# Optimization experiments

Measured on AMD Instinct MI355X. Metric: run time of the kernel, lower is better.

## Reference

```python
import jax, jax.numpy as jnp
import numpy as np

N, D, H, DH = 8192, 512, 8, 64          # seq len, model dim, heads, head dim
NF = int(DH * math_log) if False else 266  # nb_features = int(64 * ln(64)) = 266
EPS = 1e-4                               # performer softmax-kernel eps
LN_EPS = 1e-5


def layernorm(x, g, b):
    mu = x.mean(-1, keepdims=True)
    var = ((x - mu) ** 2).mean(-1, keepdims=True)
    return (x - mu) * jax.lax.rsqrt(var + LN_EPS) * g + b


def softmax_kernel(data, proj, is_query):
    # data: [b,h,n,dh], proj: [nf,dh] -> phi(data): [b,h,n,nf]
    dnorm = DH ** -0.25
    ratio = NF ** -0.5
    dd = jnp.einsum('bhnd,jd->bhnj', data * dnorm, proj)
    diag = (data ** 2).sum(-1, keepdims=True) * 0.5 * (dnorm ** 2)
    if is_query:
        m = jnp.max(dd, axis=-1, keepdims=True)
    else:
        m = jnp.max(dd, axis=(-1, -2), keepdims=True)
    return ratio * (jnp.exp(dd - diag - m) + EPS)


def setup_inputs() -> dict:
    key = jax.random.key(0)
    ks = jax.random.split(key, 10)
    s = 0.02
    return {
        'x': jax.random.normal(ks[0], (N, D), jnp.float32),
        'proj': jax.random.normal(ks[1], (NF, DH), jnp.float32),
        'ln1_g': jnp.ones((D,), jnp.float32), 'ln1_b': jnp.zeros((D,), jnp.float32),
        'wq': jax.random.normal(ks[2], (D, D), jnp.float32) * s,
        'wk': jax.random.normal(ks[3], (D, D), jnp.float32) * s,
        'wv': jax.random.normal(ks[4], (D, D), jnp.float32) * s,
        'wo': jax.random.normal(ks[5], (D, D), jnp.float32) * s,
        'wo_b': jnp.zeros((D,), jnp.float32),
        'ln2_g': jnp.ones((D,), jnp.float32), 'ln2_b': jnp.zeros((D,), jnp.float32),
        'w1': jax.random.normal(ks[6], (D, 4 * D), jnp.float32) * s,
        'b1': jnp.zeros((4 * D,), jnp.float32),
        'w2': jax.random.normal(ks[7], (4 * D, D), jnp.float32) * s,
        'b2': jnp.zeros((D,), jnp.float32),
    }


def reference(x, proj, ln1_g, ln1_b, wq, wk, wv, wo, wo_b, ln2_g, ln2_b, w1, b1, w2, b2):
    xb = x[None]                                     # [1,N,D] (the unsqueeze(0))
    # --- PreLN FAVOR+ self-attention ---
    h = layernorm(xb, ln1_g, ln1_b)
    def split_heads(t):
        return t.reshape(1, N, H, DH).transpose(0, 2, 1, 3)   # [1,H,N,DH]
    q = split_heads(h @ wq)
    k = split_heads(h @ wk)
    v = split_heads(h @ wv)
    qp = softmax_kernel(q, proj, True)               # [1,H,N,NF]
    kp = softmax_kernel(k, proj, False)              # [1,H,N,NF]
    # non-causal linear attention
    context = jnp.einsum('bhnj,bhnd->bhjd', kp, v)   # [1,H,NF,DH]
    d_inv = 1.0 / jnp.einsum('bhnj,bhj->bhn', qp, kp.sum(axis=2))
    attn = jnp.einsum('bhnj,bhjd->bhnd', qp, context) * d_inv[..., None]
    attn = attn.transpose(0, 2, 1, 3).reshape(1, N, D)
    xb = xb + attn @ wo + wo_b
    # --- PreLN feed-forward (GELU, mult=4) ---
    h2 = layernorm(xb, ln2_g, ln2_b)
    xb = xb + jax.nn.gelu(h2 @ w1 + b1) @ w2 + b2
    return xb[0]                                     # squeeze -> [N,D]
```

## Files before the change

### kernel.cpp

```cpp
#include <hip/hip_runtime.h>
#include <math.h>


typedef __attribute__((ext_vector_type(8))) short bf16x8;
typedef __attribute__((ext_vector_type(4))) float f32x4;

#define N_SEQ 8192
#define DMODEL 512
#define DQKV 1536
#define NHEAD 8
#define DHEAD 64
#define NF 266
#define NFP 320
#define PEPS 1e-4f
#define LNEPS 1e-5f
#define RATIO 0.06131393694f

__device__ __forceinline__ unsigned short f2bf(float f) {
  unsigned u = __float_as_uint(f);
  u += 0x7FFFu + ((u >> 16) & 1u);
  return (unsigned short)(u >> 16);
}
__device__ __forceinline__ float bf2f(unsigned short b) {
  return __uint_as_float(((unsigned)b) << 16);
}
__device__ __forceinline__ unsigned enc_f32(float f) {
  unsigned i = __float_as_uint(f);
  return (i & 0x80000000u) ? ~i : (i | 0x80000000u);
}
__device__ __forceinline__ float dec_f32(unsigned u) {
  return (u & 0x80000000u) ? __uint_as_float(u & 0x7FFFFFFFu) : __uint_as_float(~u);
}

__device__ __forceinline__ void g2l16(const void* g, void* l) {
  __builtin_amdgcn_global_load_lds(
      (const __attribute__((address_space(1))) void*)g,
      (__attribute__((address_space(3))) void*)l, 16, 0, 0);
}

template <int N>
__device__ __forceinline__ void wait_vmcnt() {
  if constexpr (N == 0) asm volatile("s_waitcnt vmcnt(0)" ::: "memory");
  else if constexpr (N == 6) asm volatile("s_waitcnt vmcnt(6)" ::: "memory");
  else if constexpr (N == 12) asm volatile("s_waitcnt vmcnt(12)" ::: "memory");
}
__device__ __forceinline__ void wait_lgkm0() {
  asm volatile("s_waitcnt lgkmcnt(0)" ::: "memory");
}


__global__ __launch_bounds__(256) void prep_kernel(
    const float* __restrict__ wq, const float* __restrict__ wk,
    const float* __restrict__ wv, const float* __restrict__ wo,
    const float* __restrict__ w1, const float* __restrict__ w2,
    const float* __restrict__ proj,
    unsigned short* __restrict__ wtqkv, unsigned short* __restrict__ wot,
    unsigned short* __restrict__ w1t, unsigned short* __restrict__ w2t,
    unsigned short* __restrict__ pb, unsigned* __restrict__ mk) {
  int bid = blockIdx.x;
  if (bid < 3072) {
    const float* src; unsigned short* dst; int R, C, base;
    if (bid < 256)       { src = wq; dst = wtqkv;          R = 512;  C = 512;  base = 0; }
    else if (bid < 512)  { src = wk; dst = wtqkv + 262144; R = 512;  C = 512;  base = 256; }
    else if (bid < 768)  { src = wv; dst = wtqkv + 524288; R = 512;  C = 512;  base = 512; }
    else if (bid < 1024) { src = wo; dst = wot;            R = 512;  C = 512;  base = 768; }
    else if (bid < 2048) { src = w1; dst = w1t;            R = 512;  C = 2048; base = 1024; }
    else                 { src = w2; dst = w2t;            R = 2048; C = 512;  base = 2048; }
    int lb = bid - base;
    int nbx = C / 32;
    int c0 = (lb % nbx) * 32, r0 = (lb / nbx) * 32;
    __shared__ float tile[32][33];
    int tx = threadIdx.x & 31, ty = threadIdx.x >> 5;
    #pragma unroll
    for (int i = ty; i < 32; i += 8)
      tile[i][tx] = src[(long)(r0 + i) * C + c0 + tx];
    __syncthreads();
    #pragma unroll
    for (int i = ty; i < 32; i += 8)
      dst[(long)(c0 + i) * R + r0 + tx] = f2bf(tile[tx][i]);
  } else if (bid < 3152) {
    int id = (bid - 3072) * 256 + threadIdx.x;
    int j = id >> 6;
    pb[id] = (j < NF) ? f2bf(proj[(long)j * 64 + (id & 63)] * 0.35355339059327373f)
                      : (unsigned short)0;
  } else {
    if (threadIdx.x < NHEAD) mk[threadIdx.x] = 0x007FFFFFu;
  }
}


__global__ __launch_bounds__(256) void ln_kernel(const float* __restrict__ x,
                                                 const float* __restrict__ g,
                                                 const float* __restrict__ b,
                                                 unsigned short* __restrict__ out) {
  __shared__ float sred[4];
  int row = blockIdx.x, t = threadIdx.x;
  float2 v = ((const float2*)(x + (long)row * DMODEL))[t];
  float s = v.x + v.y;
  #pragma unroll
  for (int m = 32; m >= 1; m >>= 1) s += __shfl_xor(s, m);
  if ((t & 63) == 0) sred[t >> 6] = s;
  __syncthreads();
  float mu = (sred[0] + sred[1] + sred[2] + sred[3]) * (1.0f / DMODEL);
  __syncthreads();
  float d0 = v.x - mu, d1 = v.y - mu;
  float q = d0 * d0 + d1 * d1;
  #pragma unroll
  for (int m = 32; m >= 1; m >>= 1) q += __shfl_xor(q, m);
  if ((t & 63) == 0) sred[t >> 6] = q;
  __syncthreads();
  float var = (sred[0] + sred[1] + sred[2] + sred[3]) * (1.0f / DMODEL);
  float inv = rsqrtf(var + LNEPS);
  int c = t * 2;
  unsigned short o0 = f2bf(d0 * inv * g[c] + b[c]);
  unsigned short o1 = f2bf(d1 * inv * g[c + 1] + b[c + 1]);
  ((unsigned*)(out + (long)row * DMODEL))[t] = ((unsigned)o1 << 16) | o0;
}

enum { EPI_BF16 = 0, EPI_BIAS_RES_F32 = 2, EPI_BIAS_GELU = 3, EPI_QKV = 4 };


template <int BM, int BN, int WM, int WN, int EPI>
__global__ __launch_bounds__(256) void gemm_kernel(
    const unsigned short* __restrict__ A, int lda,
    const unsigned short* __restrict__ Bt, int ldb,
    void* __restrict__ Cv, int ldc,
    int K,
    const float* __restrict__ bias,
    const float* __restrict__ res, int ldr,
    unsigned short* __restrict__ vt) {
  static_assert((BM / WM) * (BN / WN) == 4, "need 4 waves");
  constexpr int MR = WM / 16, NR = WN / 16;
  constexpr int WNN = BN / WN;
  constexpr int AIT = BM * 8 / 256;
  constexpr int BIT = BN * 8 / 256;
  constexpr int S = AIT + BIT;
  const int tid = threadIdx.x;
  const int wave = tid >> 6, lane = tid & 63;
  const int lr = lane & 15, lg = lane >> 4;
  const int wr = wave / WNN, wc = wave % WNN;
  const int m0 = blockIdx.x * BM, n0 = blockIdx.y * BN;

  __shared__ uint4 a_s[2][BM * 8];
  __shared__ uint4 b_s[2][BN * 8];

  const unsigned short* asrc[AIT];
  #pragma unroll
  for (int e = 0; e < AIT; ++e) {
    int chunk = e * 256 + tid;
    int r = chunk >> 3, c = chunk & 7;
    asrc[e] = A + (long)(m0 + r) * lda + (c ^ (r & 7)) * 8;
  }
  const unsigned short* bsrc[BIT];
  #pragma unroll
  for (int e = 0; e < BIT; ++e) {
    int chunk = e * 256 + tid;
    int r = chunk >> 3, c = chunk & 7;
    bsrc[e] = Bt + (long)(n0 + r) * ldb + (c ^ (r & 7)) * 8;
  }
  const int wbase = tid & 192;

  f32x4 acc[MR][NR] = {};

  auto stage = [&](int buf, int t) {
    #pragma unroll
    for (int e = 0; e < AIT; ++e)
      g2l16(asrc[e] + t * 64, &a_s[buf][e * 256 + wbase]);
    #pragma unroll
    for (int e = 0; e < BIT; ++e)
      g2l16(bsrc[e] + t * 64, &b_s[buf][e * 256 + wbase]);
  };
  auto compute = [&](int buf) {
    #pragma unroll
    for (int ks = 0; ks < 2; ++ks) {
      bf16x8 af[MR], bv[NR];
      #pragma unroll
      for (int i = 0; i < MR; ++i) {
        int r = wr * WM + i * 16 + lr;
        af[i] = *(const bf16x8*)&a_s[buf][r * 8 + ((ks * 4 + lg) ^ (r & 7))];
      }
      #pragma unroll
      for (int j = 0; j < NR; ++j) {
        int r = wc * WN + j * 16 + lr;
        bv[j] = *(const bf16x8*)&b_s[buf][r * 8 + ((ks * 4 + lg) ^ (r & 7))];
      }
      #pragma unroll
      for (int i = 0; i < MR; ++i)
        #pragma unroll
        for (int j = 0; j < NR; ++j)
          acc[i][j] = __builtin_amdgcn_mfma_f32_16x16x32_bf16(af[i], bv[j], acc[i][j], 0, 0, 0);
    }
  };

  const int NT = K >> 6;
  stage(0, 0);
  stage(1, 1);
  wait_vmcnt<S>();
  __builtin_amdgcn_s_barrier();

  int cur = 0;
  for (int t = 0; t < NT; ++t) {
    compute(cur);
    if (t + 1 < NT) {
      wait_lgkm0();
      __builtin_amdgcn_s_barrier();
      if (t + 2 < NT) {
        stage(cur, t + 2);
        wait_vmcnt<S>();
      } else {
        wait_vmcnt<0>();
      }
      __builtin_amdgcn_s_barrier();
    }
    cur ^= 1;
  }

  #pragma unroll
  for (int i = 0; i < MR; ++i) {
    #pragma unroll
    for (int j = 0; j < NR; ++j) {
      int gn = n0 + wc * WN + j * 16 + lr;
      int gm0 = m0 + wr * WM + i * 16 + lg * 4;
      if (EPI == EPI_QKV && gn >= 1024) {
        int d = gn - 1024;
        uint2 u;
        u.x = (unsigned)f2bf(acc[i][j][0]) | ((unsigned)f2bf(acc[i][j][1]) << 16);
        u.y = (unsigned)f2bf(acc[i][j][2]) | ((unsigned)f2bf(acc[i][j][3]) << 16);
        *(uint2*)(vt + (long)d * N_SEQ + gm0) = u;
        continue;
      }
      #pragma unroll
      for (int rg = 0; rg < 4; ++rg) {
        int gm = gm0 + rg;
        float v = acc[i][j][rg];
        if (EPI == EPI_BF16 || EPI == EPI_QKV) {
          ((unsigned short*)Cv)[(long)gm * ldc + gn] = f2bf(v);
        } else if (EPI == EPI_BIAS_RES_F32) {
          v += bias[gn] + res[(long)gm * ldr + gn];
          ((float*)Cv)[(long)gm * ldc + gn] = v;
        } else if (EPI == EPI_BIAS_GELU) {
          v += bias[gn];
          float t3 = 0.7978845608028654f * (v + 0.044715f * v * v * v);
          v = v / (1.0f + __expf(-2.0f * t3));
          ((unsigned short*)Cv)[(long)gm * ldc + gn] = f2bf(v);
        }
      }
    }
  }
}


__global__ __launch_bounds__(256) void kmax_kernel(
    const unsigned short* __restrict__ Kp,
    const unsigned short* __restrict__ pb,
    unsigned* __restrict__ mk) {
  const int tid = threadIdx.x;
  const int wave = tid >> 6, lane = tid & 63;
  const int lr = lane & 15, lg = lane >> 4;
  const int h = blockIdx.z;
  const int m0 = blockIdx.x * 64;

  __shared__ uint4 a_s4[512];
  __shared__ uint4 b_s4[2560];
  __shared__ float sred[4];

  const unsigned short* Aq = Kp + (long)m0 * DQKV + h * DHEAD;
  const int wbase = tid & 192;

  #pragma unroll
  for (int e = 0; e < 2; ++e) {
    int chunk = e * 256 + tid;
    int r = chunk >> 3, c = chunk & 7;
    g2l16(Aq + (long)r * DQKV + (c ^ (r & 7)) * 8, a_s4 + e * 256 + wbase);
  }
  #pragma unroll
  for (int e = 0; e < 10; ++e) {
    int chunk = e * 256 + tid;
    int r = chunk >> 3, c = chunk & 7;
    g2l16(pb + (long)r * DHEAD + (c ^ (r & 7)) * 8, b_s4 + e * 256 + wbase);
  }
  __syncthreads();

  f32x4 acc[17] = {};
  #pragma unroll
  for (int ks = 0; ks < 2; ++ks) {
    int rA = wave * 16 + lr;
    bf16x8 af = *(const bf16x8*)&a_s4[rA * 8 + ((ks * 4 + lg) ^ (rA & 7))];
    #pragma unroll
    for (int j = 0; j < 17; ++j) {
      int rB = j * 16 + lr;
      bf16x8 bv = *(const bf16x8*)&b_s4[rB * 8 + ((ks * 4 + lg) ^ (rB & 7))];
      acc[j] = __builtin_amdgcn_mfma_f32_16x16x32_bf16(af, bv, acc[j], 0, 0, 0);
    }
  }

  float m = -3.0e38f;
  #pragma unroll
  for (int j = 0; j < 17; ++j) {
    bool valid = (j < 16) || (lr < 10);
    if (valid) {
      #pragma unroll
      for (int rg = 0; rg < 4; ++rg) m = fmaxf(m, acc[j][rg]);
    }
  }
  #pragma unroll
  for (int s = 1; s < 64; s <<= 1) m = fmaxf(m, __shfl_xor(m, s));
  if (lane == 0) sred[wave] = m;
  __syncthreads();
  if (tid == 0) {
    float mm = fmaxf(fmaxf(sred[0], sred[1]), fmaxf(sred[2], sred[3]));
    atomicMax(&mk[h], enc_f32(mm));
  }
}


__global__ __launch_bounds__(256) void ctx_fused_kernel(
    const unsigned short* __restrict__ Kp,
    const unsigned short* __restrict__ pb,
    const unsigned short* __restrict__ vT,
    const unsigned* __restrict__ mk,
    float* __restrict__ part,
    float* __restrict__ kspart) {
  const int tid = threadIdx.x;
  const int wave = tid >> 6, lane = tid & 63;
  const int lr = lane & 15, lg = lane >> 4;
  const int kc = blockIdx.x, h = blockIdx.y;
  const int wbase = tid & 192;

  __shared__ uint4 smem[7168];
  uint4* pbs = smem;
  auto kbuf = [&](int b) { return smem + 2560 + b * 512; };
  auto vbuf = [&](int b) { return smem + 3584 + b * 512; };
  uint4* Pt = smem + 4608;

  #pragma unroll
  for (int e = 0; e < 10; ++e) {
    int chunk = e * 256 + tid;
    int r = chunk >> 3, c = chunk & 7;
    g2l16(pb + (long)r * DHEAD + (c ^ (r & 7)) * 8, pbs + e * 256 + wbase);
  }

  auto stage_kv = [&](int b, int sub) {
    int n0 = kc * 256 + sub * 64;
    #pragma unroll
    for (int e = 0; e < 2; ++e) {
      int chunk = e * 256 + tid;
      int r = chunk >> 3, c = chunk & 7;
      g2l16(Kp + (long)(n0 + r) * DQKV + h * DHEAD + (c ^ (r & 7)) * 8,
            kbuf(b) + e * 256 + wbase);
      g2l16(vT + ((long)h * DHEAD + r) * N_SEQ + n0 + (c ^ (r & 7)) * 8,
            vbuf(b) + e * 256 + wbase);
    }
  };

  const float mh = dec_f32(mk[h]);
  f32x4 acc2[2][10] = {};
  float colacc[20];
  #pragma unroll
  for (int j = 0; j < 20; ++j) colacc[j] = 0.f;

  const int wr = wave >> 1, wc = wave & 1;

  stage_kv(0, 0);
  for (int sub = 0; sub < 4; ++sub) {
    const int cur = sub & 1;
    __syncthreads();
    if (sub + 1 < 4) stage_kv(cur ^ 1, sub + 1);

    f32x4 acc[20] = {};
    float qs = 0.f;
    #pragma unroll
    for (int ks = 0; ks < 2; ++ks) {
      int rA = wave * 16 + lr;
      bf16x8 af = *(const bf16x8*)&kbuf(cur)[rA * 8 + ((ks * 4 + lg) ^ (rA & 7))];
      #pragma unroll
      for (int i = 0; i < 8; ++i) {
        float f = bf2f((unsigned short)af[i]);
        qs += f * f;
      }
      #pragma unroll
      for (int j = 0; j < 20; ++j) {
        int rB = j * 16 + lr;
        bf16x8 bv = *(const bf16x8*)&pbs[rB * 8 + ((ks * 4 + lg) ^ (rB & 7))];
        acc[j] = __builtin_amdgcn_mfma_f32_16x16x32_bf16(af, bv, acc[j], 0, 0, 0);
      }
    }
    qs += __shfl_xor(qs, 16);
    qs += __shfl_xor(qs, 32);
    float dg[4];
    #pragma unroll
    for (int rg = 0; rg < 4; ++rg) dg[rg] = 0.0625f * __shfl(qs, lg * 4 + rg);

    __syncthreads();

    unsigned short* Ptu = (unsigned short*)Pt;
    const int nrow = wave * 16 + lg * 4;
    #pragma unroll
    for (int j = 0; j < 20; ++j) {
      int colj = j * 16 + lr;
      #pragma unroll
      for (int rg = 0; rg < 4; ++rg) {
        float v = 0.f;
        if (colj < NF) v = RATIO * (__expf(acc[j][rg] - dg[rg] - mh) + PEPS);
        colacc[j] += v;
        int nr = nrow + rg;
        int idx = ((colj * 8 + ((nr >> 3) ^ (colj & 7))) << 3) + (nr & 7);
        Ptu[idx] = f2bf(v);
      }
    }
    __syncthreads();

    #pragma unroll
    for (int ks = 0; ks < 2; ++ks) {
      bf16x8 af[2], bv[10];
      #pragma unroll
      for (int i = 0; i < 2; ++i) {
        int r = wr * 32 + i * 16 + lr;
        af[i] = *(const bf16x8*)&vbuf(cur)[r * 8 + ((ks * 4 + lg) ^ (r & 7))];
      }
      #pragma unroll
      for (int j = 0; j < 10; ++j) {
        int r = wc * 160 + j * 16 + lr;
        bv[j] = *(const bf16x8*)&Pt[r * 8 + ((ks * 4 + lg) ^ (r & 7))];
      }
      #pragma unroll
      for (int i = 0; i < 2; ++i)
        #pragma unroll
        for (int j = 0; j < 10; ++j)
          acc2[i][j] = __builtin_amdgcn_mfma_f32_16x16x32_bf16(af[i], bv[j], acc2[i][j], 0, 0, 0);
    }
  }

  float* pbase = part + ((long)(h * 32 + kc)) * 64 * NFP;
  #pragma unroll
  for (int i = 0; i < 2; ++i) {
    #pragma unroll
    for (int j = 0; j < 10; ++j) {
      int gn = wc * 160 + j * 16 + lr;
      #pragma unroll
      for (int rg = 0; rg < 4; ++rg) {
        int gm = wr * 32 + i * 16 + lg * 4 + rg;
        pbase[(long)gm * NFP + gn] = acc2[i][j][rg];
      }
    }
  }

  __syncthreads();
  float* kls = (float*)Pt;
  #pragma unroll
  for (int j = 0; j < 20; ++j) {
    float cs = colacc[j];
    cs += __shfl_xor(cs, 16);
    cs += __shfl_xor(cs, 32);
    if (lg == 0) kls[wave * NFP + j * 16 + lr] = cs;
  }
  __syncthreads();
  for (int c0 = tid; c0 < NFP; c0 += 256) {
    kspart[((long)(h * 32 + kc)) * NFP + c0] =
        kls[c0] + kls[NFP + c0] + kls[2 * NFP + c0] + kls[3 * NFP + c0];
  }
}


__global__ void ctx_reduce_kernel(const float* __restrict__ part,
                                  const float* __restrict__ kspart,
                                  unsigned short* __restrict__ ctxpad) {
  int i = blockIdx.x * 256 + threadIdx.x;
  int h = i / (96 * NFP);
  int rem = i % (96 * NFP);
  int r = rem / NFP, j = rem % NFP;
  float s = 0.f;
  if (r < 64) {
    #pragma unroll 4
    for (int kc = 0; kc < 32; ++kc)
      s += part[((long)(h * 32 + kc)) * 64 * NFP + r * NFP + j];
  } else if (r == 64) {
    #pragma unroll 4
    for (int kc = 0; kc < 32; ++kc)
      s += kspart[((long)(h * 32 + kc)) * NFP + j];
  }
  ctxpad[i] = f2bf(s);
}


__global__ __launch_bounds__(256) void attn_fused_kernel(
    const unsigned short* __restrict__ Qp,
    const unsigned short* __restrict__ pb,
    const unsigned short* __restrict__ ctxpad,
    unsigned short* __restrict__ attn) {
  const int tid = threadIdx.x;
  const int wave = tid >> 6, lane = tid & 63;
  const int lr = lane & 15, lg = lane >> 4;
  const int h = blockIdx.z;
  const int m0 = blockIdx.x * 64;
  const int wbase = tid & 192;

  __shared__ uint4 smem[4096];
  auto sbuf = [&](int b) { return smem + b * 768; };
  uint4* Pf = smem + 1536;

  const unsigned short* Aq = Qp + (long)m0 * DQKV + h * DHEAD;
  const unsigned short* Ch = ctxpad + (long)h * 96 * NFP;

  auto stage_ctx = [&](int b, int kk) {
    #pragma unroll
    for (int e = 0; e < 3; ++e) {
      int chunk = e * 256 + tid;
      int r = chunk >> 3, c = chunk & 7;
      g2l16(Ch + (long)r * NFP + kk * 64 + (c ^ (r & 7)) * 8, sbuf(b) + e * 256 + wbase);
    }
  };

  #pragma unroll
  for (int e = 0; e < 2; ++e) {
    int chunk = e * 256 + tid;
    int r = chunk >> 3, c = chunk & 7;
    g2l16(Aq + (long)r * DQKV + (c ^ (r & 7)) * 8, sbuf(0) + e * 256 + wbase);
  }
  #pragma unroll
  for (int e = 0; e < 10; ++e) {
    int chunk = e * 256 + tid;
    int r = chunk >> 3, c = chunk & 7;
    g2l16(pb + (long)r * DHEAD + (c ^ (r & 7)) * 8, Pf + e * 256 + wbase);
  }
  __syncthreads();

  f32x4 acc[20] = {};
  float qs = 0.f;
  #pragma unroll
  for (int ks = 0; ks < 2; ++ks) {
    int rA = wave * 16 + lr;
    bf16x8 af = *(const bf16x8*)&sbuf(0)[rA * 8 + ((ks * 4 + lg) ^ (rA & 7))];
    #pragma unroll
    for (int i = 0; i < 8; ++i) {
      float f = bf2f((unsigned short)af[i]);
      qs += f * f;
    }
    #pragma unroll
    for (int j = 0; j < 20; ++j) {
      int rB = j * 16 + lr;
      bf16x8 bv = *(const bf16x8*)&Pf[rB * 8 + ((ks * 4 + lg) ^ (rB & 7))];
      acc[j] = __builtin_amdgcn_mfma_f32_16x16x32_bf16(af, bv, acc[j], 0, 0, 0);
    }
  }
  qs += __shfl_xor(qs, 16);
  qs += __shfl_xor(qs, 32);
  float dg[4];
  #pragma unroll
  for (int rg = 0; rg < 4; ++rg) dg[rg] = 0.0625f * __shfl(qs, lg * 4 + rg);

  float mrow[4];
  #pragma unroll
  for (int rg = 0; rg < 4; ++rg) mrow[rg] = -3.0e38f;
  #pragma unroll
  for (int j = 0; j < 17; ++j) {
    bool valid = (j < 16) || (lr < 10);
    if (valid) {
      #pragma unroll
      for (int rg = 0; rg < 4; ++rg) mrow[rg] = fmaxf(mrow[rg], acc[j][rg]);
    }
  }
  #pragma unroll
  for (int s = 1; s < 16; s <<= 1)
    #pragma unroll
    for (int rg = 0; rg < 4; ++rg) mrow[rg] = fmaxf(mrow[rg], __shfl_xor(mrow[rg], s));

  __syncthreads();
  stage_ctx(0, 0);

  unsigned short* Pu = (unsigned short*)Pf;
  const int prow = wave * 16 + lg * 4;
  #pragma unroll
  for (int j = 0; j < 20; ++j) {
    int col = j * 16 + lr;
    int kk = col >> 6, cc = (col >> 3) & 7;
    #pragma unroll
    for (int rg = 0; rg < 4; ++rg) {
      float v = 0.f;
      if (col < NF) v = RATIO * (__expf(acc[j][rg] - dg[rg] - mrow[rg]) + PEPS);
      int rw = prow + rg;
      int idx = ((kk * 512 + rw * 8 + (cc ^ (rw & 7))) << 3) + (col & 7);
      Pu[idx] = f2bf(v);
    }
  }
  __syncthreads();

  f32x4 acc2[6] = {};
  #pragma unroll
  for (int kk = 0; kk < 5; ++kk) {
    const int cur = kk & 1;
    if (kk + 1 < 5) stage_ctx(cur ^ 1, kk + 1);
    #pragma unroll
    for (int ks = 0; ks < 2; ++ks) {
      int rA = wave * 16 + lr;
      bf16x8 af = *(const bf16x8*)&Pf[kk * 512 + rA * 8 + ((ks * 4 + lg) ^ (rA & 7))];
      #pragma unroll
      for (int j = 0; j < 6; ++j) {
        int rB = j * 16 + lr;
        bf16x8 bv = *(const bf16x8*)&sbuf(cur)[rB * 8 + ((ks * 4 + lg) ^ (rB & 7))];
        acc2[j] = __builtin_amdgcn_mfma_f32_16x16x32_bf16(af, bv, acc2[j], 0, 0, 0);
      }
    }
    if (kk + 1 < 5) __syncthreads();
  }

  #pragma unroll
  for (int rg = 0; rg < 4; ++rg) {
    float dv = __shfl(acc2[4][rg], lane & 48);
    float inv = 1.0f / dv;
    int gm = m0 + wave * 16 + lg * 4 + rg;
    #pragma unroll
    for (int j = 0; j < 4; ++j) {
      attn[(long)gm * DMODEL + h * DHEAD + j * 16 + lr] = f2bf(acc2[j][rg] * inv);
    }
  }
}


extern "C" void kernel_launch(void* const* d_in, const int* in_sizes, int n_in,
                              void* d_out, int out_size, void* d_ws, size_t ws_size,
                              hipStream_t stream) {
  const float* x    = (const float*)d_in[0];
  const float* proj = (const float*)d_in[1];
  const float* ln1g = (const float*)d_in[2];
  const float* ln1b = (const float*)d_in[3];
  const float* wq   = (const float*)d_in[4];
  const float* wk   = (const float*)d_in[5];
  const float* wv   = (const float*)d_in[6];
  const float* wo   = (const float*)d_in[7];
  const float* wob  = (const float*)d_in[8];
  const float* ln2g = (const float*)d_in[9];
  const float* ln2b = (const float*)d_in[10];
  const float* w1   = (const float*)d_in[11];
  const float* b1   = (const float*)d_in[12];
  const float* w2   = (const float*)d_in[13];
  const float* b2   = (const float*)d_in[14];

  char* ws = (char*)d_ws;
  unsigned short* wtqkv = (unsigned short*)(ws + 0);
  unsigned short* wot   = (unsigned short*)(ws + 1572864);
  unsigned short* w1t   = (unsigned short*)(ws + 2097152);
  unsigned short* w2t   = (unsigned short*)(ws + 4194304);
  unsigned short* pb    = (unsigned short*)(ws + 6291456);
  unsigned short* h_bf  = (unsigned short*)(ws + 6332416);
  unsigned short* qkv   = (unsigned short*)(ws + 14721024);
  unsigned* mk          = (unsigned*)(ws + 124297216);
  unsigned short* vT    = (unsigned short*)(ws + 124297472);
  float* part           = (float*)(ws + 132686080);
  float* kspart         = (float*)(ws + 153657600);
  unsigned short* ctxpad= (unsigned short*)(ws + 154978560);
  unsigned short* gbf   = (unsigned short*)(ws + 130468096);
  unsigned short* attn  = h_bf;
  unsigned short* h2    = qkv;
  float* xb             = (float*)d_out;

  dim3 blk(256);

  prep_kernel<<<3153, blk, 0, stream>>>(wq, wk, wv, wo, w1, w2, proj,
                                        wtqkv, wot, w1t, w2t, pb, mk);

  ln_kernel<<<N_SEQ, blk, 0, stream>>>(x, ln1g, ln1b, h_bf);

  gemm_kernel<128, 64, 64, 32, EPI_QKV><<<dim3(64, 24), blk, 0, stream>>>(
      h_bf, 512, wtqkv, 512, qkv, DQKV, 512, nullptr, nullptr, 0, vT);

  kmax_kernel<<<dim3(128, 1, 8), blk, 0, stream>>>(qkv + 512, pb, mk);

  ctx_fused_kernel<<<dim3(32, 8), blk, 0, stream>>>(qkv + 512, pb, vT, mk, part, kspart);
  ctx_reduce_kernel<<<960, blk, 0, stream>>>(part, kspart, ctxpad);

  attn_fused_kernel<<<dim3(128, 1, 8), blk, 0, stream>>>(qkv, pb, ctxpad, attn);

  gemm_kernel<128, 64, 64, 32, EPI_BIAS_RES_F32><<<dim3(64, 8), blk, 0, stream>>>(
      attn, 512, wot, 512, xb, 512, 512, wob, x, 512, nullptr);

  ln_kernel<<<N_SEQ, blk, 0, stream>>>(xb, ln2g, ln2b, h2);

  gemm_kernel<128, 64, 64, 32, EPI_BIAS_GELU><<<dim3(64, 32), blk, 0, stream>>>(
      h2, 512, w1t, 512, gbf, 2048, 512, b1, nullptr, 0, nullptr);

  gemm_kernel<128, 64, 64, 32, EPI_BIAS_RES_F32><<<dim3(64, 8), blk, 0, stream>>>(
      gbf, 2048, w2t, 2048, d_out, 512, 2048, b2, xb, 512, nullptr);
}
```

Baseline: 185.5 us.

## Add 256x256-tile 8-wave GEMM for QKV and FFN-up projections

Introduces a new GEMM kernel with 256x256 output tiles, 512 threads (8 waves, each computing 128x64), double-buffered direct global-to-LDS loads interleaved with the MFMA k-steps, and s_setprio around the MFMA bursts. It replaces the 128x64-tile kernel for the QKV projection and the FFN first layer, aiming for higher arithmetic intensity per loaded byte and fewer, larger blocks. The risk is low block counts (192 and 256 blocks) against the CU count, plus heavy register pressure from 32 accumulators per wave. The old GEMM loses its QKV epilogue and uses a fixed vmcnt wait.

```diff
diff --git a/kernel.cpp b/kernel.cpp
--- a/kernel.cpp
+++ b/kernel.cpp
@@ -41,8 +41,7 @@
 template <int N>
 __device__ __forceinline__ void wait_vmcnt() {
   if constexpr (N == 0) asm volatile("s_waitcnt vmcnt(0)" ::: "memory");
-  else if constexpr (N == 6) asm volatile("s_waitcnt vmcnt(6)" ::: "memory");
-  else if constexpr (N == 12) asm volatile("s_waitcnt vmcnt(12)" ::: "memory");
+  else if constexpr (N == 8) asm volatile("s_waitcnt vmcnt(8)" ::: "memory");
 }
 __device__ __forceinline__ void wait_lgkm0() {
   asm volatile("s_waitcnt lgkmcnt(0)" ::: "memory");
@@ -120,6 +119,122 @@
 enum { EPI_BF16 = 0, EPI_BIAS_RES_F32 = 2, EPI_BIAS_GELU = 3, EPI_QKV = 4 };
 
 
+template <int EPI>
+__global__ __launch_bounds__(512, 1) void gemm8p_kernel(
+    const unsigned short* __restrict__ A, int lda,
+    const unsigned short* __restrict__ Bt, int ldb,
+    void* __restrict__ Cv, int ldc,
+    int K,
+    const float* __restrict__ bias,
+    unsigned short* __restrict__ vt) {
+  constexpr int MR = 8, NR = 4;
+  const int tid = threadIdx.x;
+  const int wave = tid >> 6, lane = tid & 63;
+  const int lr = lane & 15, lg = lane >> 4;
+  const int wr = wave >> 2, wc = wave & 3;
+  const int m0 = blockIdx.x * 256, n0 = blockIdx.y * 256;
+
+  __shared__ uint4 a_s[2][2048];
+  __shared__ uint4 b_s[2][2048];
+
+  const unsigned short* asrc[4];
+  const unsigned short* bsrc[4];
+  #pragma unroll
+  for (int e = 0; e < 4; ++e) {
+    int chunk = e * 512 + tid;
+    int r = chunk >> 3, c = chunk & 7;
+    asrc[e] = A + (long)(m0 + r) * lda + (c ^ (r & 7)) * 8;
+    bsrc[e] = Bt + (long)(n0 + r) * ldb + (c ^ (r & 7)) * 8;
+  }
+  const int wbase = tid & 448;
+
+  f32x4 acc[MR][NR] = {};
+
+  auto stage_a = [&](int buf, int t) {
+    #pragma unroll
+    for (int e = 0; e < 4; ++e)
+      g2l16(asrc[e] + t * 64, &a_s[buf][e * 512 + wbase]);
+  };
+  auto stage_b = [&](int buf, int t) {
+    #pragma unroll
+    for (int e = 0; e < 4; ++e)
+      g2l16(bsrc[e] + t * 64, &b_s[buf][e * 512 + wbase]);
+  };
+  auto compute_ks = [&](int buf, int ks) {
+    bf16x8 af[MR], bv[NR];
+    #pragma unroll
+    for (int i = 0; i < MR; ++i) {
+      int r = wr * 128 + i * 16 + lr;
+      af[i] = *(const bf16x8*)&a_s[buf][r * 8 + ((ks * 4 + lg) ^ (r & 7))];
+    }
+    #pragma unroll
+    for (int j = 0; j < NR; ++j) {
+      int r = wc * 64 + j * 16 + lr;
+      bv[j] = *(const bf16x8*)&b_s[buf][r * 8 + ((ks * 4 + lg) ^ (r & 7))];
+    }
+    __builtin_amdgcn_s_setprio(1);
+    #pragma unroll
+    for (int i = 0; i < MR; ++i)
+      #pragma unroll
+      for (int j = 0; j < NR; ++j)
+        acc[i][j] = __builtin_amdgcn_mfma_f32_16x16x32_bf16(af[i], bv[j], acc[i][j], 0, 0, 0);
+    __builtin_amdgcn_s_setprio(0);
+  };
+
+  const int NT = K >> 6;
+  stage_a(0, 0);
+  stage_b(0, 0);
+  wait_vmcnt<0>();
+  __builtin_amdgcn_s_barrier();
+
+  for (int t = 0; t < NT; ++t) {
+    const int cur = t & 1;
+    const bool more = (t + 1 < NT);
+    if (more) stage_a(cur ^ 1, t + 1);
+    compute_ks(cur, 0);
+    if (more) stage_b(cur ^ 1, t + 1);
+    compute_ks(cur, 1);
+    if (more) {
+      wait_lgkm0();
+      __builtin_amdgcn_sched_barrier(0);
+      __builtin_amdgcn_s_barrier();
+      wait_vmcnt<0>();
+      __builtin_amdgcn_s_barrier();
+    }
+  }
+
+  #pragma unroll
+  for (int i = 0; i < MR; ++i) {
+    #pragma unroll
+    for (int j = 0; j < NR; ++j) {
+      int gn = n0 + wc * 64 + j * 16 + lr;
+      int gm0 = m0 + wr * 128 + i * 16 + lg * 4;
+      if (EPI == EPI_QKV && gn >= 1024) {
+        int d = gn - 1024;
+        uint2 u;
+        u.x = (unsigned)f2bf(acc[i][j][0]) | ((unsigned)f2bf(acc[i][j][1]) << 16);
+        u.y = (unsigned)f2bf(acc[i][j][2]) | ((unsigned)f2bf(acc[i][j][3]) << 16);
+        *(uint2*)(vt + (long)d * N_SEQ + gm0) = u;
+        continue;
+      }
+      #pragma unroll
+      for (int rg = 0; rg < 4; ++rg) {
+        int gm = gm0 + rg;
+        float v = acc[i][j][rg];
+        if (EPI == EPI_BF16 || EPI == EPI_QKV) {
+          ((unsigned short*)Cv)[(long)gm * ldc + gn] = f2bf(v);
+        } else if (EPI == EPI_BIAS_GELU) {
+          v += bias[gn];
+          float t3 = 0.7978845608028654f * (v + 0.044715f * v * v * v);
+          v = v / (1.0f + __expf(-2.0f * t3));
+          ((unsigned short*)Cv)[(long)gm * ldc + gn] = f2bf(v);
+        }
+      }
+    }
+  }
+}
+
+
 template <int BM, int BN, int WM, int WN, int EPI>
 __global__ __launch_bounds__(256) void gemm_kernel(
     const unsigned short* __restrict__ A, int lda,
@@ -127,14 +242,12 @@
     void* __restrict__ Cv, int ldc,
     int K,
     const float* __restrict__ bias,
-    const float* __restrict__ res, int ldr,
-    unsigned short* __restrict__ vt) {
+    const float* __restrict__ res, int ldr) {
   static_assert((BM / WM) * (BN / WN) == 4, "need 4 waves");
   constexpr int MR = WM / 16, NR = WN / 16;
   constexpr int WNN = BN / WN;
   constexpr int AIT = BM * 8 / 256;
   constexpr int BIT = BN * 8 / 256;
-  constexpr int S = AIT + BIT;
   const int tid = threadIdx.x;
   const int wave = tid >> 6, lane = tid & 63;
   const int lr = lane & 15, lg = lane >> 4;
@@ -195,7 +308,7 @@
   const int NT = K >> 6;
   stage(0, 0);
   stage(1, 1);
-  wait_vmcnt<S>();
+  wait_vmcnt<8>();
   __builtin_amdgcn_s_barrier();
 
   int cur = 0;
@@ -206,7 +319,7 @@
       __builtin_amdgcn_s_barrier();
       if (t + 2 < NT) {
         stage(cur, t + 2);
-        wait_vmcnt<S>();
+        wait_vmcnt<8>();
       } else {
         wait_vmcnt<0>();
       }
@@ -220,20 +333,11 @@
     #pragma unroll
     for (int j = 0; j < NR; ++j) {
       int gn = n0 + wc * WN + j * 16 + lr;
-      int gm0 = m0 + wr * WM + i * 16 + lg * 4;
-      if (EPI == EPI_QKV && gn >= 1024) {
-        int d = gn - 1024;
-        uint2 u;
-        u.x = (unsigned)f2bf(acc[i][j][0]) | ((unsigned)f2bf(acc[i][j][1]) << 16);
-        u.y = (unsigned)f2bf(acc[i][j][2]) | ((unsigned)f2bf(acc[i][j][3]) << 16);
-        *(uint2*)(vt + (long)d * N_SEQ + gm0) = u;
-        continue;
-      }
       #pragma unroll
       for (int rg = 0; rg < 4; ++rg) {
-        int gm = gm0 + rg;
+        int gm = m0 + wr * WM + i * 16 + lg * 4 + rg;
         float v = acc[i][j][rg];
-        if (EPI == EPI_BF16 || EPI == EPI_QKV) {
+        if (EPI == EPI_BF16) {
           ((unsigned short*)Cv)[(long)gm * ldc + gn] = f2bf(v);
         } else if (EPI == EPI_BIAS_RES_F32) {
           v += bias[gn] + res[(long)gm * ldr + gn];
@@ -661,8 +765,8 @@
 
   ln_kernel<<<N_SEQ, blk, 0, stream>>>(x, ln1g, ln1b, h_bf);
 
-  gemm_kernel<128, 64, 64, 32, EPI_QKV><<<dim3(64, 24), blk, 0, stream>>>(
-      h_bf, 512, wtqkv, 512, qkv, DQKV, 512, nullptr, nullptr, 0, vT);
+  gemm8p_kernel<EPI_QKV><<<dim3(32, 6), dim3(512), 0, stream>>>(
+      h_bf, 512, wtqkv, 512, qkv, DQKV, 512, nullptr, vT);
 
   kmax_kernel<<<dim3(128, 1, 8), blk, 0, stream>>>(qkv + 512, pb, mk);
 
@@ -672,13 +776,13 @@
   attn_fused_kernel<<<dim3(128, 1, 8), blk, 0, stream>>>(qkv, pb, ctxpad, attn);
 
   gemm_kernel<128, 64, 64, 32, EPI_BIAS_RES_F32><<<dim3(64, 8), blk, 0, stream>>>(
-      attn, 512, wot, 512, xb, 512, 512, wob, x, 512, nullptr);
+      attn, 512, wot, 512, xb, 512, 512, wob, x, 512);
 
   ln_kernel<<<N_SEQ, blk, 0, stream>>>(xb, ln2g, ln2b, h2);
 
-  gemm_kernel<128, 64, 64, 32, EPI_BIAS_GELU><<<dim3(64, 32), blk, 0, stream>>>(
-      h2, 512, w1t, 512, gbf, 2048, 512, b1, nullptr, 0, nullptr);
+  gemm8p_kernel<EPI_BIAS_GELU><<<dim3(32, 8), dim3(512), 0, stream>>>(
+      h2, 512, w1t, 512, gbf, 2048, 512, b1, nullptr);
 
   gemm_kernel<128, 64, 64, 32, EPI_BIAS_RES_F32><<<dim3(64, 8), blk, 0, stream>>>(
-      gbf, 2048, w2t, 2048, d_out, 512, 2048, b2, xb, 512, nullptr);
-}
+      gbf, 2048, w2t, 2048, d_out, 512, 2048, b2, xb, 512);
+}
```

Result: no change. 188.1 us (+1.4%).
